# Optimization experiments

Measured on AMD Instinct MI355X. Metric: run time of the kernel, lower is better.

Reference implementation:

```python
import jax, jax.numpy as jnp
import numpy as np

TAU = 0.1
SIGMA = 0.2
EPS = 1e-08
NUM_BINS = 128
IN_FEATURES = 512
OUT_FEATURES = 128
N = 4096
C = 16


def setup_inputs() -> dict:
    key = jax.random.key(0)
    ks = jax.random.split(key, 8)
    x1 = jax.random.normal(ks[0], (N, IN_FEATURES), dtype=jnp.float32)
    x2 = jax.random.normal(ks[1], (N, IN_FEATURES), dtype=jnp.float32)
    y1 = jax.random.randint(ks[2], (N,), 0, C, dtype=jnp.int32)
    y2 = jax.random.randint(ks[3], (N,), 0, C, dtype=jnp.int32)
    W1 = jax.random.normal(ks[4], (IN_FEATURES, OUT_FEATURES), dtype=jnp.float32) * 0.02
    b1 = jnp.zeros((OUT_FEATURES,), dtype=jnp.float32)
    W2 = jax.random.normal(ks[5], (OUT_FEATURES, OUT_FEATURES), dtype=jnp.float32) * 0.02
    b2 = jnp.zeros((OUT_FEATURES,), dtype=jnp.float32)
    bins = jnp.linspace(-5.0, 5.0, NUM_BINS).astype(jnp.float32)
    return {"input_embeddings_1": x1, "y1": y1, "input_embeddings_2": x2, "y2": y2,
            "W1": W1, "b1": b1, "W2": W2, "b2": b2, "bins": bins, "num_classes": C}


def _marginal_pdf(x_norm, bins):
    # x_norm: (b, D) L2-normalized rows; bins: (num_bins,)
    # residuals: (b, D, num_bins) -- dominant memory-bound intermediate
    kernel = jnp.exp(-0.5 * ((x_norm[:, :, None] - bins[None, None, :]) / SIGMA) ** 2)
    pdf = kernel.mean(axis=1)                         # (b, num_bins)
    pdf = pdf / (pdf.sum(axis=1, keepdims=True) + EPS)
    return jax.nn.softmax(pdf, axis=-1)


def _get_distribution(x, y, bins, num_classes):
    # x: (b, out_features) projected embeddings
    x_norm = x / jnp.linalg.norm(x, axis=1, keepdims=True)
    pdf = _marginal_pdf(x_norm, bins)                 # (b, num_bins)
    sums = jax.ops.segment_sum(pdf, y, num_segments=num_classes)
    counts = jax.ops.segment_sum(jnp.ones((y.shape[0],), pdf.dtype), y, num_segments=num_classes)
    return sums / counts[:, None]                     # (C, num_bins) per-class mean pdf


def _kld_matrix(A, M):
    P = jnp.concatenate([A, M], axis=0)               # (2C, num_bins)
    logP = jnp.log(P)
    inter = jnp.sum(P[:, None, :] * (logP[:, None, :] - logP[None, :, :]), axis=-1)
    n = P.shape[0]
    return inter * (1.0 - jnp.eye(n, dtype=P.dtype))


def reference(input_embeddings_1, y1, input_embeddings_2, y2, W1, b1, W2, b2, bins, num_classes):
    def proj(x):
        h = jax.nn.relu(x @ W1 + b1)
        return h @ W2 + b2

    dA = _get_distribution(proj(input_embeddings_1), y1, bins, num_classes)
    dB = _get_distribution(proj(input_embeddings_2), y2, bins, num_classes)
    M = 0.5 * (dA + dB)
    J = 0.5 * (_kld_matrix(dA, M) + _kld_matrix(dB, M))  # (2C, 2C)
    div_ij = jnp.diagonal(J, offset=num_classes)
    div_ji = jnp.diagonal(J, offset=-num_classes)
    positives = jnp.concatenate([div_ij, div_ji], axis=0)
    nominator = jnp.exp(positives / TAU)
    denominator = jnp.sum(jnp.exp(J / TAU), axis=1)
    partial_loss = -jnp.log(nominator / denominator)
    return jnp.mean(partial_loss)
```

## Files before the change

### kernel.cpp

```cpp
#include <hip/hip_runtime.h>
#include <hip/hip_bf16.h>

#define NROWS 4096
#define IN_F 512
#define OUT_F 128
#define NBINS 128
#define NCLS 16
#define EPSV 1e-8f
#define TAUV 0.1f

#define C2EXP (-18.0336880f)
#define INV_STEP (12.7f)
#define WRAD 17

#if defined(__has_builtin)
#if __has_builtin(__builtin_amdgcn_exp2f)
#define EXP2F(x) __builtin_amdgcn_exp2f(x)
#else
#define EXP2F(x) exp2f(x)
#endif
#else
#define EXP2F(x) exp2f(x)
#endif

typedef __attribute__((ext_vector_type(8))) short bf16x8;
typedef __attribute__((ext_vector_type(4))) float f32x4;

__device__ __forceinline__ short cvt_bf16(float x) {
    __hip_bfloat16 h = __float2bfloat16(x);
    return *reinterpret_cast<short*>(&h);
}
__device__ __forceinline__ float bf_to_f(unsigned short u) {
    return __uint_as_float((unsigned int)u << 16);
}

__global__ __launch_bounds__(128) void prep_w(
    const float* __restrict__ W1, const float* __restrict__ W2,
    __hip_bfloat16* __restrict__ W1T, __hip_bfloat16* __restrict__ W2T)
{
    const int n = blockIdx.x;
    const int t = threadIdx.x;
    for (int k = t; k < IN_F; k += 128)
        W1T[(size_t)n * IN_F + k] = __float2bfloat16(W1[(size_t)k * OUT_F + n]);
    W2T[(size_t)n * OUT_F + t] = __float2bfloat16(W2[(size_t)t * OUT_F + n]);
}

__global__ __launch_bounds__(512) void fused_proj_pdf(
    const float* __restrict__ X1, const float* __restrict__ X2,
    const __hip_bfloat16* __restrict__ W1T, const float* __restrict__ b1,
    const __hip_bfloat16* __restrict__ W2T, const float* __restrict__ b2,
    const float* __restrict__ bins, __hip_bfloat16* __restrict__ SM)
{
    __shared__ __hip_bfloat16 xb[16][IN_F + 8];
    __shared__ __hip_bfloat16 h_lds[16][136];
    __shared__ float pout[16][128];
    __shared__ float rowX[8][2][128];
    __shared__ float bins_s[NBINS];
    const int tid  = threadIdx.x;
    const int wave = tid >> 6;
    const int lane = tid & 63;
    const int lr   = lane & 15;
    const int kg   = lane >> 4;
    const int row0 = blockIdx.x * 16;
    const float* __restrict__ X = (row0 < NROWS) ? X1 : X2;
    const int xr0 = (row0 < NROWS) ? row0 : row0 - NROWS;
    const int col = wave * 16 + lr;

    if (tid < NBINS) bins_s[tid] = bins[tid];

    for (int i = tid; i < 16 * 128; i += 512) {
        const int r = i >> 7, c4 = i & 127;
        float4 v = *reinterpret_cast<const float4*>(
            X + (size_t)(xr0 + r) * IN_F + c4 * 4);
        short4 s;
        s.x = cvt_bf16(v.x); s.y = cvt_bf16(v.y);
        s.z = cvt_bf16(v.z); s.w = cvt_bf16(v.w);
        *reinterpret_cast<short4*>(&xb[r][c4 * 4]) = s;
    }
    __syncthreads();

    f32x4 acc = {0.f, 0.f, 0.f, 0.f};
    {
        const __hip_bfloat16* __restrict__ wrow = W1T + (size_t)col * IN_F;
        #pragma unroll 4
        for (int ks = 0; ks < IN_F / 32; ++ks) {
            const int kb = ks * 32 + kg * 8;
            bf16x8 a = *reinterpret_cast<const bf16x8*>(&xb[lr][kb]);
            bf16x8 b = *reinterpret_cast<const bf16x8*>(wrow + kb);
            acc = __builtin_amdgcn_mfma_f32_16x16x32_bf16(a, b, acc, 0, 0, 0);
        }
    }
    {
        const float bb = b1[col];
        #pragma unroll
        for (int q = 0; q < 4; ++q)
            h_lds[kg * 4 + q][col] = __float2bfloat16(fmaxf(acc[q] + bb, 0.f));
    }
    __syncthreads();

    f32x4 c2 = {0.f, 0.f, 0.f, 0.f};
    {
        const __hip_bfloat16* __restrict__ w2row = W2T + (size_t)col * OUT_F;
        #pragma unroll
        for (int ks = 0; ks < OUT_F / 32; ++ks) {
            const int kb = ks * 32 + kg * 8;
            bf16x8 a2 = *reinterpret_cast<const bf16x8*>(&h_lds[lr][kb]);
            bf16x8 b2f = *reinterpret_cast<const bf16x8*>(w2row + kb);
            c2 = __builtin_amdgcn_mfma_f32_16x16x32_bf16(a2, b2f, c2, 0, 0, 0);
        }
    }
    {
        const float cb = b2[col];
        #pragma unroll
        for (int q = 0; q < 4; ++q)
            pout[kg * 4 + q][col] = c2[q] + cb;
    }
    __syncthreads();

    const int m0 = wave * 2, m1 = m0 + 1;

    const float p00 = pout[m0][lane], p01 = pout[m0][lane + 64];
    const float p10 = pout[m1][lane], p11 = pout[m1][lane + 64];

    float s0 = p00 * p00 + p01 * p01;
    float s1 = p10 * p10 + p11 * p11;
    #pragma unroll
    for (int off = 32; off; off >>= 1) {
        s0 += __shfl_xor(s0, off);
        s1 += __shfl_xor(s1, off);
    }
    const float i0 = __frsqrt_rn(s0), i1 = __frsqrt_rn(s1);
    const float x00 = p00 * i0, x01 = p01 * i0;
    const float x10 = p10 * i1, x11 = p11 * i1;

    rowX[wave][0][lane]      = x00;
    rowX[wave][0][lane + 64] = x01;
    rowX[wave][1][lane]      = x10;
    rowX[wave][1][lane + 64] = x11;

    float xlo = fminf(fminf(x00, x01), fminf(x10, x11));
    float xhi = fmaxf(fmaxf(x00, x01), fmaxf(x10, x11));
    #pragma unroll
    for (int off = 32; off; off >>= 1) {
        xlo = fminf(xlo, __shfl_xor(xlo, off));
        xhi = fmaxf(xhi, __shfl_xor(xhi, off));
    }
    int imin = (int)floorf((xlo + 5.0f) * INV_STEP) - WRAD;
    int imax = (int)ceilf ((xhi + 5.0f) * INV_STEP) + WRAD;
    imin = imin < 0 ? 0 : (imin > 127 ? 127 : imin);
    imax = imax > 127 ? 127 : (imax < 0 ? 0 : imax);
    if (imax > imin + 63) imax = imin + 63;
    const int nact = imax - imin + 1;
    const int j = imin + lane;
    const bool act = (j <= imax);
    const float bj = bins_s[act ? j : imax];

    const float4* __restrict__ x0v = reinterpret_cast<const float4*>(&rowX[wave][0][0]);
    const float4* __restrict__ x1v = reinterpret_cast<const float4*>(&rowX[wave][1][0]);
    float aA0 = 0.f, aA1 = 0.f, aB0 = 0.f, aB1 = 0.f;
    #pragma unroll 4
    for (int q = 0; q < 32; ++q) {
        float4 u = x0v[q];
        float4 v = x1v[q];
        float t;
        t = u.x - bj; aA0 += EXP2F((C2EXP * t) * t);
        t = u.z - bj; aA1 += EXP2F((C2EXP * t) * t);
        t = v.x - bj; aB0 += EXP2F((C2EXP * t) * t);
        t = v.z - bj; aB1 += EXP2F((C2EXP * t) * t);
        t = u.y - bj; aA0 += EXP2F((C2EXP * t) * t);
        t = u.w - bj; aA1 += EXP2F((C2EXP * t) * t);
        t = v.y - bj; aB0 += EXP2F((C2EXP * t) * t);
        t = v.w - bj; aB1 += EXP2F((C2EXP * t) * t);
    }
    float pdf0 = act ? (aA0 + aA1) * (1.0f / OUT_F) : 0.f;
    float pdf1 = act ? (aB0 + aB1) * (1.0f / OUT_F) : 0.f;

    float t0 = pdf0, t1 = pdf1;
    #pragma unroll
    for (int off = 32; off; off >>= 1) {
        t0 += __shfl_xor(t0, off);
        t1 += __shfl_xor(t1, off);
    }
    pdf0 *= 1.0f / (t0 + EPSV);
    pdf1 *= 1.0f / (t1 + EPSV);

    float mx0 = pdf0, mx1 = pdf1;
    #pragma unroll
    for (int off = 32; off; off >>= 1) {
        mx0 = fmaxf(mx0, __shfl_xor(mx0, off));
        mx1 = fmaxf(mx1, __shfl_xor(mx1, off));
    }
    const float q0 = act ? __expf(pdf0 - mx0) : 0.f;
    const float q1 = act ? __expf(pdf1 - mx1) : 0.f;
    const float ez0 = __expf(-mx0), ez1 = __expf(-mx1);
    float es0 = q0, es1 = q1;
    #pragma unroll
    for (int off = 32; off; off >>= 1) {
        es0 += __shfl_xor(es0, off);
        es1 += __shfl_xor(es1, off);
    }
    es0 += (float)(NBINS - nact) * ez0;
    es1 += (float)(NBINS - nact) * ez1;
    const float r0 = 1.0f / es0, r1 = 1.0f / es1;
    const float z0 = ez0 * r0, z1 = ez1 * r1;

    const int sa = lane - imin;
    const int sb = lane + 64 - imin;
    const float w0a = __shfl(q0, sa & 63) * r0;
    const float w0b = __shfl(q0, sb & 63) * r0;
    const float w1a = __shfl(q1, sa & 63) * r1;
    const float w1b = __shfl(q1, sb & 63) * r1;
    const bool ina = (unsigned)sa < (unsigned)nact;
    const bool inb = (unsigned)sb < (unsigned)nact;

    SM[(size_t)(row0 + m0) * OUT_F + lane]      = __float2bfloat16(ina ? w0a : z0);
    SM[(size_t)(row0 + m0) * OUT_F + 64 + lane] = __float2bfloat16(inb ? w0b : z0);
    SM[(size_t)(row0 + m1) * OUT_F + lane]      = __float2bfloat16(ina ? w1a : z1);
    SM[(size_t)(row0 + m1) * OUT_F + 64 + lane] = __float2bfloat16(inb ? w1b : z1);
}

__global__ __launch_bounds__(256) void rowred_kernel(
    const __hip_bfloat16* __restrict__ SM,
    const int* __restrict__ Y1, const int* __restrict__ Y2,
    __hip_bfloat16* __restrict__ pdist, float* __restrict__ pcnt)
{
    __shared__ unsigned short rows_s[128][128];
    __shared__ int labs[128];
    const int blk = blockIdx.x;
    const int batch = blk >> 5, seg = blk & 31;
    const int tid = threadIdx.x;
    const int* __restrict__ Y = batch ? Y2 : Y1;

    {
        const unsigned short* __restrict__ src =
            (const unsigned short*)SM + ((size_t)batch * 4096 + (size_t)seg * 128) * OUT_F;
        unsigned short* dst = &rows_s[0][0];
        for (int i = tid; i < 128 * 128 / 8; i += 256) {
            *reinterpret_cast<uint4*>(dst + i * 8) =
                *reinterpret_cast<const uint4*>(src + i * 8);
        }
    }
    if (tid < 128) labs[tid] = Y[seg * 128 + tid];
    __syncthreads();

    const int jq = tid & 31;
    const int c0 = tid >> 5;
    f32x4 acc0 = {0.f, 0.f, 0.f, 0.f};
    f32x4 acc1 = {0.f, 0.f, 0.f, 0.f};
    int cnt0 = 0, cnt1 = 0;
    for (int r = 0; r < 128; ++r) {
        ushort4 v = *reinterpret_cast<const ushort4*>(&rows_s[r][jq * 4]);
        const float f0 = bf_to_f(v.x), f1 = bf_to_f(v.y);
        const float f2 = bf_to_f(v.z), f3 = bf_to_f(v.w);
        const int lab = labs[r];
        const float h0 = (lab == c0) ? 1.f : 0.f;
        const float h1 = (lab == c0 + 8) ? 1.f : 0.f;
        acc0.x = fmaf(h0, f0, acc0.x); acc0.y = fmaf(h0, f1, acc0.y);
        acc0.z = fmaf(h0, f2, acc0.z); acc0.w = fmaf(h0, f3, acc0.w);
        acc1.x = fmaf(h1, f0, acc1.x); acc1.y = fmaf(h1, f1, acc1.y);
        acc1.z = fmaf(h1, f2, acc1.z); acc1.w = fmaf(h1, f3, acc1.w);
        cnt0 += (lab == c0);
        cnt1 += (lab == c0 + 8);
    }
    {
        unsigned short* pd = (unsigned short*)pdist;
        const size_t b0 = ((size_t)(batch * 16 + c0) * 128 + jq * 4) * 32 + seg;
        const size_t b1 = ((size_t)(batch * 16 + c0 + 8) * 128 + jq * 4) * 32 + seg;
        pd[b0 +  0] = (unsigned short)cvt_bf16(acc0.x);
        pd[b0 + 32] = (unsigned short)cvt_bf16(acc0.y);
        pd[b0 + 64] = (unsigned short)cvt_bf16(acc0.z);
        pd[b0 + 96] = (unsigned short)cvt_bf16(acc0.w);
        pd[b1 +  0] = (unsigned short)cvt_bf16(acc1.x);
        pd[b1 + 32] = (unsigned short)cvt_bf16(acc1.y);
        pd[b1 + 64] = (unsigned short)cvt_bf16(acc1.z);
        pd[b1 + 96] = (unsigned short)cvt_bf16(acc1.w);
    }
    if (jq == 0) {
        pcnt[(batch * 16 + c0) * 32 + seg]     = (float)cnt0;
        pcnt[(batch * 16 + c0 + 8) * 32 + seg] = (float)cnt1;
    }
}

__global__ __launch_bounds__(512) void final_kernel(
    const __hip_bfloat16* __restrict__ pdist, const float* __restrict__ pcnt,
    float* __restrict__ out)
{
    __shared__ float P_A[32][132], L_A[32][132];
    __shared__ float P_B[32][132], L_B[32][132];
    __shared__ float JA[32][32], JB[32][32];
    __shared__ float pls[32];
    __shared__ float cnt[32];
    __shared__ float HA[32], HB[32];
    const int tid = threadIdx.x;
    const unsigned short* __restrict__ pd = (const unsigned short*)pdist;

    if (tid < 32) {
        float s = 0.f;
        #pragma unroll 8
        for (int seg = 0; seg < 32; ++seg) s += pcnt[tid * 32 + seg];
        cnt[tid] = s;
    }

    for (int s = tid; s < 32 * NBINS; s += 512) {
        const int bc = s >> 7, jj = s & 127;
        const uint4* base = reinterpret_cast<const uint4*>(pd + (size_t)s * 32);
        float a = 0.f;
        #pragma unroll
        for (int w = 0; w < 4; ++w) {
            uint4 u = base[w];
            const unsigned short* us = (const unsigned short*)&u;
            #pragma unroll
            for (int e = 0; e < 8; ++e) a += bf_to_f(us[e]);
        }
        if (bc < 16) P_A[bc][jj] = a;
        else         P_B[bc - 16][jj] = a;
    }
    __syncthreads();

    for (int s = tid; s < NCLS * NBINS; s += 512) {
        const int c = s >> 7, jj = s & 127;
        const float a = P_A[c][jj] / cnt[c];
        const float b = P_B[c][jj] / cnt[16 + c];
        const float mm = 0.5f * (a + b);
        const float lm = __logf(mm);
        P_A[c][jj] = a;        L_A[c][jj] = __logf(a);
        P_A[c + 16][jj] = mm;  L_A[c + 16][jj] = lm;
        P_B[c][jj] = b;        L_B[c][jj] = __logf(b);
        P_B[c + 16][jj] = mm;  L_B[c + 16][jj] = lm;
    }
    __syncthreads();

    if (tid < 64) {
        const int i = tid & 31;
        const float4* Pv = reinterpret_cast<const float4*>(
            (tid < 32) ? &P_A[i][0] : &P_B[i][0]);
        const float4* Lv = reinterpret_cast<const float4*>(
            (tid < 32) ? &L_A[i][0] : &L_B[i][0]);
        float h = 0.f;
        #pragma unroll 4
        for (int q = 0; q < 32; ++q) {
            float4 p = Pv[q], l = Lv[q];
            h = fmaf(p.x, l.x, h); h = fmaf(p.y, l.y, h);
            h = fmaf(p.z, l.z, h); h = fmaf(p.w, l.w, h);
        }
        if (tid < 32) HA[i] = h; else HB[i] = h;
    }
    __syncthreads();

    if (tid < 128) {
        const int side = tid >> 6;
        const int t = tid & 63;
        const int i0 = (t >> 3) << 2, k0 = (t & 7) << 2;
        const float4* pr[4];
        const float4* lq[4];
        #pragma unroll
        for (int a = 0; a < 4; ++a) {
            pr[a] = reinterpret_cast<const float4*>(
                side ? &P_B[i0 + a][0] : &P_A[i0 + a][0]);
            lq[a] = reinterpret_cast<const float4*>(
                side ? &L_B[k0 + a][0] : &L_A[k0 + a][0]);
        }
        float accv[4][4];
        #pragma unroll
        for (int a = 0; a < 4; ++a)
            #pragma unroll
            for (int b = 0; b < 4; ++b) accv[a][b] = 0.f;
        for (int q = 0; q < 32; ++q) {
            float4 Pv[4], Lv[4];
            #pragma unroll
            for (int a = 0; a < 4; ++a) { Pv[a] = pr[a][q]; Lv[a] = lq[a][q]; }
            #pragma unroll
            for (int a = 0; a < 4; ++a)
                #pragma unroll
                for (int b = 0; b < 4; ++b) {
                    accv[a][b] = fmaf(Pv[a].x, Lv[b].x, accv[a][b]);
                    accv[a][b] = fmaf(Pv[a].y, Lv[b].y, accv[a][b]);
                    accv[a][b] = fmaf(Pv[a].z, Lv[b].z, accv[a][b]);
                    accv[a][b] = fmaf(Pv[a].w, Lv[b].w, accv[a][b]);
                }
        }
        float (*Jout)[32] = side ? JB : JA;
        #pragma unroll
        for (int a = 0; a < 4; ++a)
            #pragma unroll
            for (int b = 0; b < 4; ++b)
                Jout[i0 + a][k0 + b] = accv[a][b];
    }
    __syncthreads();

    for (int p = tid; p < 32 * 32; p += 512) {
        const int i = p >> 5, k = p & 31;
        const float Jv = (i == k) ? 0.f
            : 0.5f * ((HA[i] - JA[i][k]) + (HB[i] - JB[i][k]));
        JA[i][k] = Jv;
    }
    __syncthreads();

    if (tid < 32) {
        float den = 0.f;
        for (int k = 0; k < 32; ++k) den += __expf(JA[tid][k] * (1.0f / TAUV));
        const float pos = JA[tid][(tid + 16) & 31];
        pls[tid] = -(pos * (1.0f / TAUV)) + __logf(den);
    }
    __syncthreads();
    if (tid == 0) {
        float s = 0.f;
        for (int i = 0; i < 32; ++i) s += pls[i];
        out[0] = s * (1.0f / 32.0f);
    }
}

extern "C" void kernel_launch(void* const* d_in, const int* in_sizes, int n_in,
                              void* d_out, int out_size, void* d_ws, size_t ws_size,
                              hipStream_t stream)
{
    const float* x1   = (const float*)d_in[0];
    const int*   y1   = (const int*)d_in[1];
    const float* x2   = (const float*)d_in[2];
    const int*   y2   = (const int*)d_in[3];
    const float* W1   = (const float*)d_in[4];
    const float* b1   = (const float*)d_in[5];
    const float* W2   = (const float*)d_in[6];
    const float* b2   = (const float*)d_in[7];
    const float* bins = (const float*)d_in[8];
    float* out = (float*)d_out;

    char* ws = (char*)d_ws;
    __hip_bfloat16* SMb = (__hip_bfloat16*)ws;
    char* ws2 = ws + (size_t)8192 * 128 * 2;
    __hip_bfloat16* pdist = (__hip_bfloat16*)ws2;
    float* pcnt = (float*)(ws2 + (size_t)32 * NBINS * 32 * 2);
    __hip_bfloat16* W1T = (__hip_bfloat16*)(ws2 + (size_t)32 * NBINS * 32 * 2 + 8192);
    __hip_bfloat16* W2T = W1T + (size_t)OUT_F * IN_F;

    prep_w<<<128, 128, 0, stream>>>(W1, W2, W1T, W2T);
    fused_proj_pdf<<<512, 512, 0, stream>>>(x1, x2, W1T, b1, W2T, b2, bins, SMb);
    rowred_kernel<<<64, 256, 0, stream>>>(SMb, y1, y2, pdist, pcnt);
    final_kernel<<<1, 512, 0, stream>>>(pdist, pcnt, out);
}
```

Before: 53.59 us.

## Fuse per-class segment sum into projection kernel with partial-sum merge stage

Each projection/PDF block now keeps its 16 softmaxed rows in LDS and does its own per-class accumulation. It writes fp32 partial sums and counts per block, so the bf16 row matrix no longer goes through global memory. A new 32-block merge kernel reduces the 256 partials per batch and class, and the final kernel reads the merged distributions directly. This removes the rowred stage's global round trip and adds an LDS barrier plus roughly 4 MB of fp32 partial writes and reads.

Measured after the change: 83.19 us. +55.2%, slower.

```diff
diff --git a/kernel.cpp b/kernel.cpp
--- a/kernel.cpp
+++ b/kernel.cpp
@@ -30,9 +30,6 @@
     __hip_bfloat16 h = __float2bfloat16(x);
     return *reinterpret_cast<short*>(&h);
 }
-__device__ __forceinline__ float bf_to_f(unsigned short u) {
-    return __uint_as_float((unsigned int)u << 16);
-}
 
 __global__ __launch_bounds__(128) void prep_w(
     const float* __restrict__ W1, const float* __restrict__ W2,
@@ -47,26 +44,33 @@
 
 __global__ __launch_bounds__(512) void fused_proj_pdf(
     const float* __restrict__ X1, const float* __restrict__ X2,
+    const int* __restrict__ Y1, const int* __restrict__ Y2,
     const __hip_bfloat16* __restrict__ W1T, const float* __restrict__ b1,
     const __hip_bfloat16* __restrict__ W2T, const float* __restrict__ b2,
-    const float* __restrict__ bins, __hip_bfloat16* __restrict__ SM)
+    const float* __restrict__ bins,
+    float* __restrict__ partial, float* __restrict__ pcnt)
 {
     __shared__ __hip_bfloat16 xb[16][IN_F + 8];
     __shared__ __hip_bfloat16 h_lds[16][136];
     __shared__ float pout[16][128];
     __shared__ float rowX[8][2][128];
+    __shared__ float smrows[16][128];
     __shared__ float bins_s[NBINS];
+    __shared__ int   labs[16];
     const int tid  = threadIdx.x;
     const int wave = tid >> 6;
     const int lane = tid & 63;
     const int lr   = lane & 15;
     const int kg   = lane >> 4;
     const int row0 = blockIdx.x * 16;
-    const float* __restrict__ X = (row0 < NROWS) ? X1 : X2;
-    const int xr0 = (row0 < NROWS) ? row0 : row0 - NROWS;
+    const int batch = (row0 < NROWS) ? 0 : 1;
+    const float* __restrict__ X = batch ? X2 : X1;
+    const int* __restrict__ Y = batch ? Y2 : Y1;
+    const int xr0 = batch ? row0 - NROWS : row0;
     const int col = wave * 16 + lr;
 
     if (tid < NBINS) bins_s[tid] = bins[tid];
+    if (tid >= 128 && tid < 144) labs[tid - 128] = Y[xr0 + tid - 128];
 
     for (int i = tid; i < 16 * 128; i += 512) {
         const int r = i >> 7, c4 = i & 127;
@@ -213,76 +217,60 @@
     const bool ina = (unsigned)sa < (unsigned)nact;
     const bool inb = (unsigned)sb < (unsigned)nact;
 
-    SM[(size_t)(row0 + m0) * OUT_F + lane]      = __float2bfloat16(ina ? w0a : z0);
-    SM[(size_t)(row0 + m0) * OUT_F + 64 + lane] = __float2bfloat16(inb ? w0b : z0);
-    SM[(size_t)(row0 + m1) * OUT_F + lane]      = __float2bfloat16(ina ? w1a : z1);
-    SM[(size_t)(row0 + m1) * OUT_F + 64 + lane] = __float2bfloat16(inb ? w1b : z1);
-}
-
-__global__ __launch_bounds__(256) void rowred_kernel(
-    const __hip_bfloat16* __restrict__ SM,
-    const int* __restrict__ Y1, const int* __restrict__ Y2,
-    __hip_bfloat16* __restrict__ pdist, float* __restrict__ pcnt)
+    smrows[m0][lane]      = ina ? w0a : z0;
+    smrows[m0][lane + 64] = inb ? w0b : z0;
+    smrows[m1][lane]      = ina ? w1a : z1;
+    smrows[m1][lane + 64] = inb ? w1b : z1;
+    __syncthreads();
+
+    {
+        const int c_cls = tid >> 5;
+        const int jq    = tid & 31;
+        f32x4 accp = {0.f, 0.f, 0.f, 0.f};
+        int ccnt = 0;
+        #pragma unroll 4
+        for (int r = 0; r < 16; ++r) {
+            const float4 v = *reinterpret_cast<const float4*>(&smrows[r][jq * 4]);
+            const float h = (labs[r] == c_cls) ? 1.f : 0.f;
+            accp.x = fmaf(h, v.x, accp.x);
+            accp.y = fmaf(h, v.y, accp.y);
+            accp.z = fmaf(h, v.z, accp.z);
+            accp.w = fmaf(h, v.w, accp.w);
+            ccnt += (labs[r] == c_cls);
+        }
+        *reinterpret_cast<f32x4*>(
+            &partial[((size_t)blockIdx.x * NCLS + c_cls) * NBINS + jq * 4]) = accp;
+        if (jq == 0) pcnt[(size_t)blockIdx.x * NCLS + c_cls] = (float)ccnt;
+    }
+}
+
+__global__ __launch_bounds__(256) void merge_kernel(
+    const float* __restrict__ partial, const float* __restrict__ pcnt,
+    float* __restrict__ dist, float* __restrict__ cntg)
 {
-    __shared__ unsigned short rows_s[128][128];
-    __shared__ int labs[128];
-    const int blk = blockIdx.x;
-    const int batch = blk >> 5, seg = blk & 31;
+    __shared__ float sd[2][128];
+    __shared__ float sc[4];
+    const int bc = blockIdx.x;
+    const int batch = bc >> 4, c = bc & 15;
     const int tid = threadIdx.x;
-    const int* __restrict__ Y = batch ? Y2 : Y1;
-
-    {
-        const unsigned short* __restrict__ src =
-            (const unsigned short*)SM + ((size_t)batch * 4096 + (size_t)seg * 128) * OUT_F;
-        unsigned short* dst = &rows_s[0][0];
-        for (int i = tid; i < 128 * 128 / 8; i += 256) {
-            *reinterpret_cast<uint4*>(dst + i * 8) =
-                *reinterpret_cast<const uint4*>(src + i * 8);
-        }
-    }
-    if (tid < 128) labs[tid] = Y[seg * 128 + tid];
-    __syncthreads();
-
-    const int jq = tid & 31;
-    const int c0 = tid >> 5;
-    f32x4 acc0 = {0.f, 0.f, 0.f, 0.f};
-    f32x4 acc1 = {0.f, 0.f, 0.f, 0.f};
-    int cnt0 = 0, cnt1 = 0;
-    for (int r = 0; r < 128; ++r) {
-        ushort4 v = *reinterpret_cast<const ushort4*>(&rows_s[r][jq * 4]);
-        const float f0 = bf_to_f(v.x), f1 = bf_to_f(v.y);
-        const float f2 = bf_to_f(v.z), f3 = bf_to_f(v.w);
-        const int lab = labs[r];
-        const float h0 = (lab == c0) ? 1.f : 0.f;
-        const float h1 = (lab == c0 + 8) ? 1.f : 0.f;
-        acc0.x = fmaf(h0, f0, acc0.x); acc0.y = fmaf(h0, f1, acc0.y);
-        acc0.z = fmaf(h0, f2, acc0.z); acc0.w = fmaf(h0, f3, acc0.w);
-        acc1.x = fmaf(h1, f0, acc1.x); acc1.y = fmaf(h1, f1, acc1.y);
-        acc1.z = fmaf(h1, f2, acc1.z); acc1.w = fmaf(h1, f3, acc1.w);
-        cnt0 += (lab == c0);
-        cnt1 += (lab == c0 + 8);
-    }
-    {
-        unsigned short* pd = (unsigned short*)pdist;
-        const size_t b0 = ((size_t)(batch * 16 + c0) * 128 + jq * 4) * 32 + seg;
-        const size_t b1 = ((size_t)(batch * 16 + c0 + 8) * 128 + jq * 4) * 32 + seg;
-        pd[b0 +  0] = (unsigned short)cvt_bf16(acc0.x);
-        pd[b0 + 32] = (unsigned short)cvt_bf16(acc0.y);
-        pd[b0 + 64] = (unsigned short)cvt_bf16(acc0.z);
-        pd[b0 + 96] = (unsigned short)cvt_bf16(acc0.w);
-        pd[b1 +  0] = (unsigned short)cvt_bf16(acc1.x);
-        pd[b1 + 32] = (unsigned short)cvt_bf16(acc1.y);
-        pd[b1 + 64] = (unsigned short)cvt_bf16(acc1.z);
-        pd[b1 + 96] = (unsigned short)cvt_bf16(acc1.w);
-    }
-    if (jq == 0) {
-        pcnt[(batch * 16 + c0) * 32 + seg]     = (float)cnt0;
-        pcnt[(batch * 16 + c0 + 8) * 32 + seg] = (float)cnt1;
-    }
+    const int j = tid & 127, half = tid >> 7;
+
+    float s = 0.f;
+    for (int sb = half; sb < 256; sb += 2)
+        s += partial[((size_t)(batch * 256 + sb) * NCLS + c) * NBINS + j];
+    sd[half][j] = s;
+
+    float cv = pcnt[(size_t)(batch * 256 + tid) * NCLS + c];
+    #pragma unroll
+    for (int off = 32; off; off >>= 1) cv += __shfl_xor(cv, off);
+    if ((tid & 63) == 0) sc[tid >> 6] = cv;
+    __syncthreads();
+    if (tid < 128) dist[(size_t)bc * NBINS + tid] = sd[0][tid] + sd[1][tid];
+    if (tid == 0) cntg[bc] = sc[0] + sc[1] + sc[2] + sc[3];
 }
 
 __global__ __launch_bounds__(512) void final_kernel(
-    const __hip_bfloat16* __restrict__ pdist, const float* __restrict__ pcnt,
+    const float* __restrict__ dist, const float* __restrict__ cntg,
     float* __restrict__ out)
 {
     __shared__ float P_A[32][132], L_A[32][132];
@@ -292,35 +280,14 @@
     __shared__ float cnt[32];
     __shared__ float HA[32], HB[32];
     const int tid = threadIdx.x;
-    const unsigned short* __restrict__ pd = (const unsigned short*)pdist;
-
-    if (tid < 32) {
-        float s = 0.f;
-        #pragma unroll 8
-        for (int seg = 0; seg < 32; ++seg) s += pcnt[tid * 32 + seg];
-        cnt[tid] = s;
-    }
-
-    for (int s = tid; s < 32 * NBINS; s += 512) {
-        const int bc = s >> 7, jj = s & 127;
-        const uint4* base = reinterpret_cast<const uint4*>(pd + (size_t)s * 32);
-        float a = 0.f;
-        #pragma unroll
-        for (int w = 0; w < 4; ++w) {
-            uint4 u = base[w];
-            const unsigned short* us = (const unsigned short*)&u;
-            #pragma unroll
-            for (int e = 0; e < 8; ++e) a += bf_to_f(us[e]);
-        }
-        if (bc < 16) P_A[bc][jj] = a;
-        else         P_B[bc - 16][jj] = a;
-    }
+
+    if (tid < 32) cnt[tid] = cntg[tid];
     __syncthreads();
 
     for (int s = tid; s < NCLS * NBINS; s += 512) {
         const int c = s >> 7, jj = s & 127;
-        const float a = P_A[c][jj] / cnt[c];
-        const float b = P_B[c][jj] / cnt[16 + c];
+        const float a = dist[(size_t)c * NBINS + jj] / cnt[c];
+        const float b = dist[(size_t)(16 + c) * NBINS + jj] / cnt[16 + c];
         const float mm = 0.5f * (a + b);
         const float lm = __logf(mm);
         P_A[c][jj] = a;        L_A[c][jj] = __logf(a);
@@ -426,15 +393,16 @@
     float* out = (float*)d_out;
 
     char* ws = (char*)d_ws;
-    __hip_bfloat16* SMb = (__hip_bfloat16*)ws;
-    char* ws2 = ws + (size_t)8192 * 128 * 2;
-    __hip_bfloat16* pdist = (__hip_bfloat16*)ws2;
-    float* pcnt = (float*)(ws2 + (size_t)32 * NBINS * 32 * 2);
-    __hip_bfloat16* W1T = (__hip_bfloat16*)(ws2 + (size_t)32 * NBINS * 32 * 2 + 8192);
+    float* partial = (float*)ws;
+    float* pcnt    = (float*)(ws + (size_t)512 * NCLS * NBINS * 4);
+    float* dist    = pcnt + 512 * NCLS;
+    float* cntg    = dist + 32 * NBINS;
+    __hip_bfloat16* W1T = (__hip_bfloat16*)(cntg + 64);
     __hip_bfloat16* W2T = W1T + (size_t)OUT_F * IN_F;
 
     prep_w<<<128, 128, 0, stream>>>(W1, W2, W1T, W2T);
-    fused_proj_pdf<<<512, 512, 0, stream>>>(x1, x2, W1T, b1, W2T, b2, bins, SMb);
-    rowred_kernel<<<64, 256, 0, stream>>>(SMb, y1, y2, pdist, pcnt);
-    final_kernel<<<1, 512, 0, stream>>>(pdist, pcnt, out);
-}
+    fused_proj_pdf<<<512, 512, 0, stream>>>(x1, x2, y1, y2, W1T, b1, W2T, b2,
+                                            bins, partial, pcnt);
+    merge_kernel<<<32, 256, 0, stream>>>(partial, pcnt, dist, cntg);
+    final_kernel<<<1, 512, 0, stream>>>(dist, cntg, out);
+}
```
